# Performance work log

Hardware: AMD Instinct MI355X
Metric: run time of the kernel (lower is better)

Reference implementation:

```python
import jax, jax.numpy as jnp
import numpy as np

N = 255  # 17 * time_input(15) graph nodes


def spmm(rows, cols, vals, x):
    """Batched sparse (COO) @ dense: x is [B, N, F] -> [B, N, F]."""
    g = x[:, cols, :] * vals[None, :, None]                      # [B, nnz, F]
    out = jax.ops.segment_sum(jnp.swapaxes(g, 0, 1), rows,
                              num_segments=N)                     # [N, B, F]
    return jnp.swapaxes(out, 0, 1)


def setup_inputs() -> dict:
    key = jax.random.key(0)
    ks = jax.random.split(key, 32)
    B, nnz = 256, 2040
    inp = {"H": jax.random.normal(ks[0], (B, N, 2), jnp.float32)}
    for i, nm in enumerate(["sm_s", "sm_t", "sp_s", "sp_t"]):
        inp[nm + "_rows"] = jax.random.randint(ks[1 + 3 * i], (nnz,), 0, N, jnp.int32)
        inp[nm + "_cols"] = jax.random.randint(ks[2 + 3 * i], (nnz,), 0, N, jnp.int32)
        inp[nm + "_vals"] = jax.random.uniform(ks[3 + 3 * i], (nnz,), jnp.float32)
    dims = [(2, 400), (400, 300), (300, 100), (100, 300), (300, 400), (400, 2)]
    wnames = ["W0", "W1", "W2", "Wd0", "Wd1", "Wd2"]
    for j, (di, do) in enumerate(dims):
        inp[wnames[j]] = jax.random.normal(ks[13 + j], (di, do), jnp.float32) / np.sqrt(di).astype(np.float32)
        inp["b" + wnames[j][1:]] = jnp.zeros((do,), jnp.float32)
    return inp


def reference(H, sm_s_rows, sm_s_cols, sm_s_vals,
              sm_t_rows, sm_t_cols, sm_t_vals,
              sp_s_rows, sp_s_cols, sp_s_vals,
              sp_t_rows, sp_t_cols, sp_t_vals,
              W0, b0, W1, b1, W2, b2, Wd0, bd0, Wd1, bd1, Wd2, bd2):
    def layer(x, W, b, r, c, v):
        # Dense projection fused with Laplacian SpMM + ReLU (same math as the
        # per-sample Python loop in the original, batched over B).
        return jax.nn.relu(spmm(r, c, v, x @ W + b))

    # encoder: Laplacian smoothing (enc0, enc1 with s_DADsm; enc2 with t_DADsm)
    H = layer(H, W0, b0, sm_s_rows, sm_s_cols, sm_s_vals)
    H = layer(H, W1, b1, sm_s_rows, sm_s_cols, sm_s_vals)
    H = layer(H, W2, b2, sm_t_rows, sm_t_cols, sm_t_vals)
    # decoder: Laplacian sharpening (dec0 with t_DADsp; dec1, dec2 with s_DADsp)
    H = layer(H, Wd0, bd0, sp_t_rows, sp_t_cols, sp_t_vals)
    H = layer(H, Wd1, bd1, sp_s_rows, sp_s_cols, sp_s_vals)
    H = layer(H, Wd2, bd2, sp_s_rows, sp_s_cols, sp_s_vals)
    return H  # [B, 255, 2]
```

## Files before the change

kernel.cpp:

```cpp
#include <hip/hip_runtime.h>
#include <hip/hip_bf16.h>


#define NN 255
#define YCH 2048

typedef __attribute__((ext_vector_type(8))) short short8;
typedef __attribute__((ext_vector_type(4))) float floatx4;

__device__ __forceinline__ float bf2f(ushort u) {
    union { uint u; float f; } c; c.u = ((uint)u) << 16; return c.f;
}
__device__ __forceinline__ ushort f2bf(float f) {
    union { float f; uint u; } c; c.f = f;
    uint u = c.u + 0x7fff + ((c.u >> 16) & 1);
    return (ushort)(u >> 16);
}
__device__ __forceinline__ short8 u4_frag(uint4 v) {
    union { uint4 u; short8 s; } c; c.u = v; return c.s;
}
__device__ __forceinline__ void gl_lds16(const ushort* g, ushort* l) {
    __builtin_amdgcn_global_load_lds(
        (const __attribute__((address_space(1))) void*)g,
        (__attribute__((address_space(3))) void*)l, 16, 0, 0);
}

__global__ void zero_k(int* p, int n) {
    int i = blockIdx.x * blockDim.x + threadIdx.x;
    if (i < n) p[i] = 0;
}

__global__ void edge_k(const int* __restrict__ r0, const int* __restrict__ c0, const float* __restrict__ v0,
                       const int* __restrict__ r1, const int* __restrict__ c1, const float* __restrict__ v1,
                       const int* __restrict__ r2, const int* __restrict__ c2, const float* __restrict__ v2,
                       const int* __restrict__ r3, const int* __restrict__ c3, const float* __restrict__ v3,
                       float* Sd, float* rs, int nnz) {
    int gi = blockIdx.y;
    int e = blockIdx.x * blockDim.x + threadIdx.x;
    if (e >= nnz) return;
    const int* rr = gi == 0 ? r0 : gi == 1 ? r1 : gi == 2 ? r2 : r3;
    const int* cc = gi == 0 ? c0 : gi == 1 ? c1 : gi == 2 ? c2 : c3;
    const float* vv = gi == 0 ? v0 : gi == 1 ? v1 : gi == 2 ? v2 : v3;
    int r = rr[e], c = cc[e];
    float v = vv[e];
    atomicAdd(&Sd[gi * 65536 + r * 256 + c], v);
    atomicAdd(&rs[gi * 256 + r], v);
}

__device__ __forceinline__ void wpiece(const float* __restrict__ W, ushort* __restrict__ Wt,
                                       int K, int N, int Kpad, int idx) {
    int n = idx / Kpad, k = idx - n * Kpad;
    float v = (n < N && k < K) ? W[(size_t)k * N + n] : 0.f;
    Wt[idx] = f2bf(v);
}

__global__ void conv_k(const float* __restrict__ Sd, ushort* __restrict__ Sb,
                       const float* __restrict__ W1, ushort* __restrict__ Wt1,
                       const float* __restrict__ W2, ushort* __restrict__ Wt2,
                       const float* __restrict__ W3, ushort* __restrict__ Wt3,
                       const float* __restrict__ W4, ushort* __restrict__ Wt4) {
    int idx = blockIdx.x * blockDim.x + threadIdx.x;
    if (idx < 262144) { Sb[idx] = f2bf(Sd[idx]); return; }
    idx -= 262144;
    if (idx < 133120) { wpiece(W1, Wt1, 400, 300, 416, idx); return; }
    idx -= 133120;
    if (idx < 40960)  { wpiece(W2, Wt2, 300, 100, 320, idx); return; }
    idx -= 40960;
    if (idx < 40960)  { wpiece(W3, Wt3, 100, 300, 128, idx); return; }
    idx -= 40960;
    if (idx < 143360) { wpiece(W4, Wt4, 300, 400, 320, idx); }
}

__global__ __launch_bounds__(256) void l0_fused(const float* __restrict__ H,
                                                const float* __restrict__ Sd0,
                                                const float* __restrict__ W0,
                                                const float* __restrict__ b0,
                                                const float* __restrict__ rs0,
                                                ushort* __restrict__ Y) {
    __shared__ float hsh[512];
    __shared__ float ssh[512];
    int b = blockIdx.x, t = threadIdx.x;
    if (t < NN) {
        hsh[t * 2]     = H[((size_t)b * NN + t) * 2];
        hsh[t * 2 + 1] = H[((size_t)b * NN + t) * 2 + 1];
    } else {
        hsh[t * 2] = 0.f; hsh[t * 2 + 1] = 0.f;
    }
    __syncthreads();
    const float4* Sr = (const float4*)(Sd0 + (size_t)t * 256);
    float s0 = 0.f, s1 = 0.f;
    #pragma unroll 8
    for (int c4 = 0; c4 < 64; ++c4) {
        float4 v = Sr[c4];
        const float2* hp = (const float2*)&hsh[c4 * 8];
        float2 h0 = hp[0], h1 = hp[1], h2 = hp[2], h3 = hp[3];
        s0 = fmaf(v.x, h0.x, s0); s1 = fmaf(v.x, h0.y, s1);
        s0 = fmaf(v.y, h1.x, s0); s1 = fmaf(v.y, h1.y, s1);
        s0 = fmaf(v.z, h2.x, s0); s1 = fmaf(v.z, h2.y, s1);
        s0 = fmaf(v.w, h3.x, s0); s1 = fmaf(v.w, h3.y, s1);
    }
    ssh[t * 2] = s0; ssh[t * 2 + 1] = s1;
    __syncthreads();
    uint* out = (uint*)(Y + (((size_t)b) << 8) * 416);
    for (int i = 0; i < 200; ++i) {
        int idx = i * 256 + t;
        int m = idx / 200, n2 = idx - m * 200;
        int n = n2 * 2;
        float x0 = ssh[m * 2], x1 = ssh[m * 2 + 1];
        float rsm = rs0[m];
        float y0 = fmaf(x0, W0[n],     fmaf(x1, W0[400 + n],     rsm * b0[n]));
        float y1 = fmaf(x0, W0[n + 1], fmaf(x1, W0[400 + n + 1], rsm * b0[n + 1]));
        out[(size_t)m * 208 + n2] =
            (uint)f2bf(fmaxf(y0, 0.f)) | ((uint)f2bf(fmaxf(y1, 0.f)) << 16);
    }
}

__global__ __launch_bounds__(256, 3) void fused_layer(const ushort* __restrict__ X,
                                                      const ushort* __restrict__ Wt,
                                                      const ushort* __restrict__ Sg,
                                                      const float* __restrict__ bias,
                                                      ushort* __restrict__ Z,
                                                      int Kpad, int Nfeat, int FsN,
                                                      int nft) {
    __shared__ ushort smem[20480];
    ushort* As0 = smem;
    ushort* Bs0 = smem + 2048;
    ushort* As1 = smem + 10240;
    ushort* Bs1 = smem + 12288;
    ushort* Ys  = smem;

    int li = blockIdx.x;
    int x = li & 7, rr = li >> 3;
    int ft = rr % nft, b = (rr / nft) * 8 + x;
    int f0 = ft * 64;

    int t = threadIdx.x;
    int w = t >> 6, lane = t & 63;
    int frow = lane & 15, quad = lane >> 4;
    int rot = ((quad + (frow >> 2)) & 3) * 8;

    const ushort* Xb = X + (((size_t)b) << 8) * (size_t)Kpad;
    const ushort* gB0 = Xb + (size_t)(64 * w +  0 + (lane >> 2)) * Kpad + (lane & 3) * 8;
    const ushort* gB1 = Xb + (size_t)(64 * w + 16 + (lane >> 2)) * Kpad + (lane & 3) * 8;
    const ushort* gB2 = Xb + (size_t)(64 * w + 32 + (lane >> 2)) * Kpad + (lane & 3) * 8;
    const ushort* gB3 = Xb + (size_t)(64 * w + 48 + (lane >> 2)) * Kpad + (lane & 3) * 8;
    const ushort* gA  = Wt + (size_t)(f0 + 16 * w + (lane >> 2)) * Kpad + (lane & 3) * 8;

    floatx4 acc[4][4];
    #pragma unroll
    for (int i = 0; i < 4; ++i)
        #pragma unroll
        for (int j = 0; j < 4; ++j) acc[i][j] = (floatx4)0.f;

    int nk1 = Kpad >> 5;

    {
        ushort* Bd = Bs0 + w * 2048;
        gl_lds16(gB0, Bd);
        gl_lds16(gB1, Bd + 512);
        gl_lds16(gB2, Bd + 1024);
        gl_lds16(gB3, Bd + 1536);
        gl_lds16(gA,  As0 + w * 512);
    }
    __syncthreads();

    for (int ks = 0; ks < nk1; ++ks) {
        if (ks + 1 < nk1) {
            int off = (ks + 1) * 32;
            ushort* Asb = (ks & 1) ? As0 : As1;
            ushort* Bd  = ((ks & 1) ? Bs0 : Bs1) + w * 2048;
            gl_lds16(gB0 + off, Bd);
            gl_lds16(gB1 + off, Bd + 512);
            gl_lds16(gB2 + off, Bd + 1024);
            gl_lds16(gB3 + off, Bd + 1536);
            gl_lds16(gA  + off, Asb + w * 512);
        }
        const ushort* Asb = (ks & 1) ? As1 : As0;
        const ushort* Bsb = (ks & 1) ? Bs1 : Bs0;
        const ushort* Ab = Asb + frow * 32 + quad * 8;
        const ushort* Bb = Bsb + (w * 64 + frow) * 32 + quad * 8;
        short8 xf[4], wf[4];
        #pragma unroll
        for (int i = 0; i < 4; ++i) {
            xf[i] = u4_frag(*(const uint4*)(Bb + i * 512));
            wf[i] = u4_frag(*(const uint4*)(Ab + i * 512));
        }
        #pragma unroll
        for (int i = 0; i < 4; ++i)
            #pragma unroll
            for (int j = 0; j < 4; ++j)
                acc[i][j] = __builtin_amdgcn_mfma_f32_16x16x32_bf16(xf[i], wf[j], acc[i][j], 0, 0, 0);
        __syncthreads();
    }

    const ushort* Sp = Sg + (size_t)(w * 64 + frow) * 256 + quad * 8;
    uint4 ps[4];
    #pragma unroll
    for (int i = 0; i < 4; ++i) ps[i] = *(const uint4*)(Sp + i * 4096);

    #pragma unroll
    for (int j = 0; j < 4; ++j) {
        int f = j * 16 + frow;
        float bv = (f0 + f < Nfeat) ? bias[f0 + f] : 0.f;
        #pragma unroll
        for (int i = 0; i < 4; ++i) {
            int chunk = 2 * w + (i >> 1);
            int gc = 2 * (i & 1) + (quad >> 1);
            int base = chunk * YCH + f * 32 + (((gc + (frow >> 2)) & 3) * 8) + (quad & 1) * 4;
            uint lo = (uint)f2bf(acc[i][j][0] + bv) | ((uint)f2bf(acc[i][j][1] + bv) << 16);
            uint hi = (uint)f2bf(acc[i][j][2] + bv) | ((uint)f2bf(acc[i][j][3] + bv) << 16);
            *(uint2*)(&Ys[base]) = make_uint2(lo, hi);
        }
    }
    __syncthreads();

    #pragma unroll
    for (int i = 0; i < 4; ++i)
        #pragma unroll
        for (int j = 0; j < 4; ++j) acc[i][j] = (floatx4)0.f;

    for (int ks = 0; ks < 8; ++ks) {
        uint4 pn[4];
        if (ks < 7) {
            #pragma unroll
            for (int i = 0; i < 4; ++i)
                pn[i] = *(const uint4*)(Sp + i * 4096 + (ks + 1) * 32);
        }
        short8 bf[4];
        #pragma unroll
        for (int j = 0; j < 4; ++j)
            bf[j] = u4_frag(*(const uint4*)(&Ys[ks * YCH + (j * 16 + frow) * 32 + rot]));
        #pragma unroll
        for (int i = 0; i < 4; ++i) {
            short8 af = u4_frag(ps[i]);
            #pragma unroll
            for (int j = 0; j < 4; ++j)
                acc[i][j] = __builtin_amdgcn_mfma_f32_16x16x32_bf16(af, bf[j], acc[i][j], 0, 0, 0);
        }
        #pragma unroll
        for (int i = 0; i < 4; ++i) ps[i] = pn[i];
    }

    #pragma unroll
    for (int i = 0; i < 4; ++i)
        #pragma unroll
        for (int r = 0; r < 4; ++r) {
            int rg = w * 64 + i * 16 + quad * 4 + r;
            ushort* Zr = Z + (size_t)((b << 8) + rg) * FsN + f0;
            #pragma unroll
            for (int j = 0; j < 4; ++j)
                Zr[j * 16 + frow] = f2bf(fmaxf(acc[i][j][r], 0.f));
        }
}

__global__ __launch_bounds__(256) void l5_fused(const ushort* __restrict__ X,
                                                const float* __restrict__ Sd2,
                                                const float* __restrict__ Wd2,
                                                const float* __restrict__ bd2,
                                                float* __restrict__ out) {
    __shared__ float ysh[512];
    int b = blockIdx.x, t = threadIdx.x;
    const uint4* Xr = (const uint4*)(X + ((size_t)((b << 8) + t)) * 448);
    const float4* Wp = (const float4*)Wd2;
    float a0 = bd2[0], a1 = bd2[1];
    for (int i = 0; i < 50; ++i) {
        uint4 p = Xr[i];
        uint pv[4] = {p.x, p.y, p.z, p.w};
        #pragma unroll
        for (int q = 0; q < 4; ++q) {
            float x0 = bf2f((ushort)(pv[q] & 0xffffu));
            float x1 = bf2f((ushort)(pv[q] >> 16));
            float4 w = Wp[i * 4 + q];
            a0 = fmaf(x0, w.x, a0); a1 = fmaf(x0, w.y, a1);
            a0 = fmaf(x1, w.z, a0); a1 = fmaf(x1, w.w, a1);
        }
    }
    ysh[t * 2] = a0; ysh[t * 2 + 1] = a1;
    __syncthreads();
    if (t < NN) {
        const float4* Sr = (const float4*)(Sd2 + (size_t)t * 256);
        float s0 = 0.f, s1 = 0.f;
        #pragma unroll 8
        for (int c4 = 0; c4 < 64; ++c4) {
            float4 v = Sr[c4];
            const float2* yp = (const float2*)&ysh[c4 * 8];
            float2 y0 = yp[0], y1 = yp[1], y2 = yp[2], y3 = yp[3];
            s0 = fmaf(v.x, y0.x, s0); s1 = fmaf(v.x, y0.y, s1);
            s0 = fmaf(v.y, y1.x, s0); s1 = fmaf(v.y, y1.y, s1);
            s0 = fmaf(v.z, y2.x, s0); s1 = fmaf(v.z, y2.y, s1);
            s0 = fmaf(v.w, y3.x, s0); s1 = fmaf(v.w, y3.y, s1);
        }
        out[((size_t)b * NN + t) * 2]     = fmaxf(s0, 0.f);
        out[((size_t)b * NN + t) * 2 + 1] = fmaxf(s1, 0.f);
    }
}

extern "C" void kernel_launch(void* const* d_in, const int* in_sizes, int n_in,
                              void* d_out, int out_size, void* d_ws, size_t ws_size,
                              hipStream_t stream) {
    const float* H = (const float*)d_in[0];
    const int*   g_rows[4] = {(const int*)d_in[1], (const int*)d_in[4], (const int*)d_in[7], (const int*)d_in[10]};
    const int*   g_cols[4] = {(const int*)d_in[2], (const int*)d_in[5], (const int*)d_in[8], (const int*)d_in[11]};
    const float* g_vals[4] = {(const float*)d_in[3], (const float*)d_in[6], (const float*)d_in[9], (const float*)d_in[12]};
    const float* W0  = (const float*)d_in[13]; const float* b0  = (const float*)d_in[14];
    const float* W1  = (const float*)d_in[15]; const float* b1  = (const float*)d_in[16];
    const float* W2  = (const float*)d_in[17]; const float* b2  = (const float*)d_in[18];
    const float* Wd0 = (const float*)d_in[19]; const float* bd0 = (const float*)d_in[20];
    const float* Wd1 = (const float*)d_in[21]; const float* bd1 = (const float*)d_in[22];
    const float* Wd2 = (const float*)d_in[23]; const float* bd2 = (const float*)d_in[24];
    float* out = (float*)d_out;

    const int nnz = in_sizes[1];
    const int B   = in_sizes[0] / (NN * 2);
    const int Mp  = B * 256;

    ushort* bufA = (ushort*)d_ws;
    ushort* bufB = bufA + (size_t)Mp * 448;
    ushort* Wt1 = bufB + (size_t)Mp * 320;
    ushort* Wt2 = Wt1 + 320 * 416;
    ushort* Wt3 = Wt2 + 128 * 320;
    ushort* Wt4 = Wt3 + 320 * 128;
    ushort* Sb  = Wt4 + 448 * 320;
    float*  rs  = (float*)(Sb + 4 * 65536);
    float*  Sd  = rs + 4 * 256;
    const int ZN = 4 * 256 + 4 * 65536;

    zero_k<<<(ZN + 255) / 256, 256, 0, stream>>>((int*)rs, ZN);
    edge_k<<<dim3((nnz + 255) / 256, 4), 256, 0, stream>>>(
        g_rows[0], g_cols[0], g_vals[0], g_rows[1], g_cols[1], g_vals[1],
        g_rows[2], g_cols[2], g_vals[2], g_rows[3], g_cols[3], g_vals[3],
        Sd, rs, nnz);
    conv_k<<<(620544 + 255) / 256, 256, 0, stream>>>(Sd, Sb, W1, Wt1, W2, Wt2, Wd0, Wt3, Wd1, Wt4);

    l0_fused<<<B, 256, 0, stream>>>(H, Sd + 0 * 65536, W0, b0, rs + 0, bufA);

    fused_layer<<<B * 5, 256, 0, stream>>>(bufA, Wt1, Sb + 0 * 65536, b1, bufB, 416, 300, 320, 5);
    fused_layer<<<B * 2, 256, 0, stream>>>(bufB, Wt2, Sb + 1 * 65536, b2, bufA, 320, 100, 128, 2);
    fused_layer<<<B * 5, 256, 0, stream>>>(bufA, Wt3, Sb + 3 * 65536, bd0, bufB, 128, 300, 320, 5);
    fused_layer<<<B * 7, 256, 0, stream>>>(bufB, Wt4, Sb + 2 * 65536, bd1, bufA, 320, 400, 448, 7);

    l5_fused<<<B, 256, 0, stream>>>(bufA, Sd + 2 * 65536, Wd2, bd2, out);
}
```

Before: 348.0 us.

## Deepen GEMM k-loop prefetch to two stages with manual waitcnt barriers

Restructures the fused_layer k-loop so global-to-LDS loads are issued two iterations ahead instead of one. The shared W tile becomes triple-buffered, while each wave's private X tile stays double-buffered and is refilled right after its fragments are read into registers. The full __syncthreads is replaced by explicit vmcnt/lgkmcnt waits plus s_barrier, so loads can stay in flight across the barrier. The aim is to hide more global-load latency behind MFMA work, at the cost of extra LDS and fragile hand-tuned wait counts.

New measurement: 342.1 us. Within noise of the previous version (-1.7%).

```diff
diff --git a/kernel.cpp b/kernel.cpp
--- a/kernel.cpp
+++ b/kernel.cpp
@@ -122,11 +122,12 @@
                                                       ushort* __restrict__ Z,
                                                       int Kpad, int Nfeat, int FsN,
                                                       int nft) {
-    __shared__ ushort smem[20480];
+    __shared__ ushort smem[22528];
     ushort* As0 = smem;
-    ushort* Bs0 = smem + 2048;
-    ushort* As1 = smem + 10240;
-    ushort* Bs1 = smem + 12288;
+    ushort* As1 = smem + 2048;
+    ushort* As2 = smem + 4096;
+    ushort* Bs0 = smem + 6144;
+    ushort* Bs1 = smem + 14336;
     ushort* Ys  = smem;
 
     int li = blockIdx.x;
@@ -156,41 +157,54 @@
 
     {
         ushort* Bd = Bs0 + w * 2048;
-        gl_lds16(gB0, Bd);
-        gl_lds16(gB1, Bd + 512);
-        gl_lds16(gB2, Bd + 1024);
-        gl_lds16(gB3, Bd + 1536);
+        gl_lds16(gB0, Bd);        gl_lds16(gB1, Bd + 512);
+        gl_lds16(gB2, Bd + 1024); gl_lds16(gB3, Bd + 1536);
         gl_lds16(gA,  As0 + w * 512);
-    }
-    __syncthreads();
+        ushort* Bd1 = Bs1 + w * 2048;
+        gl_lds16(gB0 + 32, Bd1);        gl_lds16(gB1 + 32, Bd1 + 512);
+        gl_lds16(gB2 + 32, Bd1 + 1024); gl_lds16(gB3 + 32, Bd1 + 1536);
+        gl_lds16(gA  + 32, As1 + w * 512);
+    }
+    __builtin_amdgcn_sched_barrier(0);
+    asm volatile("s_waitcnt vmcnt(5)" ::: "memory");
+    __builtin_amdgcn_s_barrier();
+    __builtin_amdgcn_sched_barrier(0);
+
+    ushort *a0 = As0, *a1 = As1, *a2 = As2;
+    ushort *bc = Bs0, *bn = Bs1;
 
     for (int ks = 0; ks < nk1; ++ks) {
-        if (ks + 1 < nk1) {
-            int off = (ks + 1) * 32;
-            ushort* Asb = (ks & 1) ? As0 : As1;
-            ushort* Bd  = ((ks & 1) ? Bs0 : Bs1) + w * 2048;
-            gl_lds16(gB0 + off, Bd);
-            gl_lds16(gB1 + off, Bd + 512);
-            gl_lds16(gB2 + off, Bd + 1024);
-            gl_lds16(gB3 + off, Bd + 1536);
-            gl_lds16(gA  + off, Asb + w * 512);
-        }
-        const ushort* Asb = (ks & 1) ? As1 : As0;
-        const ushort* Bsb = (ks & 1) ? Bs1 : Bs0;
-        const ushort* Ab = Asb + frow * 32 + quad * 8;
-        const ushort* Bb = Bsb + (w * 64 + frow) * 32 + quad * 8;
+        const ushort* Ab = a0 + frow * 32 + quad * 8;
+        const ushort* Bb = bc + (w * 64 + frow) * 32 + quad * 8;
         short8 xf[4], wf[4];
         #pragma unroll
         for (int i = 0; i < 4; ++i) {
             xf[i] = u4_frag(*(const uint4*)(Bb + i * 512));
             wf[i] = u4_frag(*(const uint4*)(Ab + i * 512));
+        }
+        asm volatile("s_waitcnt lgkmcnt(0)" ::: "memory");
+        __builtin_amdgcn_sched_barrier(0);
+        if (ks + 2 < nk1) {
+            int off = (ks + 2) * 32;
+            ushort* Bd = bc + w * 2048;
+            gl_lds16(gB0 + off, Bd);        gl_lds16(gB1 + off, Bd + 512);
+            gl_lds16(gB2 + off, Bd + 1024); gl_lds16(gB3 + off, Bd + 1536);
+            gl_lds16(gA  + off, a2 + w * 512);
         }
         #pragma unroll
         for (int i = 0; i < 4; ++i)
             #pragma unroll
             for (int j = 0; j < 4; ++j)
                 acc[i][j] = __builtin_amdgcn_mfma_f32_16x16x32_bf16(xf[i], wf[j], acc[i][j], 0, 0, 0);
-        __syncthreads();
+        __builtin_amdgcn_sched_barrier(0);
+        if (ks + 2 < nk1)
+            asm volatile("s_waitcnt vmcnt(5)" ::: "memory");
+        else
+            asm volatile("s_waitcnt vmcnt(0)" ::: "memory");
+        __builtin_amdgcn_s_barrier();
+        __builtin_amdgcn_sched_barrier(0);
+        ushort* ta = a0; a0 = a1; a1 = a2; a2 = ta;
+        ushort* tb = bc; bc = bn; bn = tb;
     }
 
     const ushort* Sp = Sg + (size_t)(w * 64 + frow) * 256 + quad * 8;
```
